# Kernel optimization log

Measured on AMD Instinct MI355X. Metric: run time of the kernel, lower is better.

The kernel has to match this reference:

```python
import jax, jax.numpy as jnp
import numpy as np

B, N, H = 8, 256, 128
EDGE_IN = 2 * H + 1
NODE_IN = 2 * H


def _glorot(key, shape):
    fan_in, fan_out = shape[0], shape[1]
    lim = 1.0 / np.sqrt(fan_in)
    return jax.random.uniform(key, shape, jnp.float32, -lim, lim)


def setup_inputs() -> dict:
    key = jax.random.key(0)
    ks = jax.random.split(key, 12)
    node_state = jax.random.normal(ks[0], (B, N, H), jnp.float32)
    positions = jax.random.normal(ks[1], (B, N, 3), jnp.float32)
    mask = jnp.ones((B, N), jnp.float32)
    # edge_mlp: Linear(2H+1 -> H), SiLU, Linear(H -> H)  (weights stored [in, out])
    We1 = _glorot(ks[2], (EDGE_IN, H)); be1 = _glorot(ks[3], (1, H))[0]
    We2 = _glorot(ks[4], (H, H));       be2 = _glorot(ks[5], (1, H))[0]
    # node_mlp: Linear(2H -> H), SiLU, Linear(H -> H)
    Wn1 = _glorot(ks[6], (NODE_IN, H)); bn1 = _glorot(ks[7], (1, H))[0]
    Wn2 = _glorot(ks[8], (H, H));       bn2 = _glorot(ks[9], (1, H))[0]
    return {"node_state": node_state, "positions": positions, "mask": mask,
            "We1": We1, "be1": be1, "We2": We2, "be2": be2,
            "Wn1": Wn1, "bn1": bn1, "Wn2": Wn2, "bn2": bn2}


def reference(node_state, positions, mask, We1, be1, We2, be2, Wn1, bn1, Wn2, bn2):
    b, n, h = node_state.shape
    # pairwise distances [B, N, N, 1]; safe-sqrt so grad at i==j is 0 (exact fwd)
    rel = positions[:, :, None, :] - positions[:, None, :, :]
    sq = jnp.sum(rel * rel, axis=-1, keepdims=True)
    dist = jnp.where(sq > 0, jnp.sqrt(jnp.where(sq > 0, sq, 1.0)), 0.0)
    # broadcast-concat node features for all pairs -> [B, N, N, 2H+1]
    node_i = jnp.broadcast_to(node_state[:, :, None, :], (b, n, n, h))
    node_j = jnp.broadcast_to(node_state[:, None, :, :], (b, n, n, h))
    edge_input = jnp.concatenate([node_i, node_j, dist], axis=-1)
    edge_msg = jax.nn.silu(edge_input @ We1 + be1) @ We2 + be2  # [B,N,N,H]
    # pairwise validity mask [B, N, N, 1]
    edge_mask = (mask[:, None, :] * mask[:, :, None])[..., None]
    edge_msg = edge_msg * edge_mask
    # masked mean over j
    denom = jnp.clip(jnp.sum(edge_mask, axis=2), 1.0, None)  # [B,N,1]
    aggregated = jnp.sum(edge_msg, axis=2) / denom           # [B,N,H]
    node_in = jnp.concatenate([node_state, aggregated], axis=-1)
    updated = jax.nn.silu(node_in @ Wn1 + bn1) @ Wn2 + bn2
    return node_state + updated * mask[..., None]
```

## Files before the change

kernel.cpp:

```cpp
#include <hip/hip_runtime.h>
#include <hip/hip_bf16.h>
#include <math.h>

#define B_ 8
#define N_ 256
#define H_ 128
#define NODES_ (B_ * N_)

__device__ __forceinline__ float silu_fast(float x) {
    float e = __expf(-x);
    return x * __builtin_amdgcn_rcpf(1.0f + e);
}

__global__ __launch_bounds__(512) void k1(
    const float* __restrict__ node, const float* __restrict__ We1,
    const float* __restrict__ be1, const float* __restrict__ Wn1,
    const float* __restrict__ bn1, const float* __restrict__ mask,
    float* __restrict__ P, float* __restrict__ Q, float* __restrict__ pre)
{
    __shared__ __align__(16) float act[4][128];
    __shared__ __align__(16) float pls[16][4][128];
    const int t = threadIdx.x;
    const int g = blockIdx.x >> 9;
    const int node0 = (blockIdx.x & 511) * 4;

    if (t < 128) {
        int r = t >> 5, col = (t & 31) * 4;
        *(float4*)(&act[r][col]) = *(const float4*)(node + (size_t)(node0 + r) * H_ + col);
    }
    const float* W = (g == 0) ? We1 : (g == 1) ? (We1 + 128 * H_) : Wn1;
    const int kseg = t >> 5;
    const int c0   = (t & 31) * 4;
    __syncthreads();

    float4 w[8];
    const float* Wb = W + (size_t)(kseg * 8) * H_ + c0;
    #pragma unroll
    for (int u = 0; u < 8; ++u) w[u] = *(const float4*)(Wb + u * H_);

    #pragma unroll
    for (int n = 0; n < 4; ++n) {
        float4 a = {0.f, 0.f, 0.f, 0.f};
        #pragma unroll
        for (int u = 0; u < 8; ++u) {
            float v = act[n][kseg * 8 + u];
            a.x = fmaf(v, w[u].x, a.x);
            a.y = fmaf(v, w[u].y, a.y);
            a.z = fmaf(v, w[u].z, a.z);
            a.w = fmaf(v, w[u].w, a.w);
        }
        *(float4*)(&pls[kseg][n][c0]) = a;
    }
    __syncthreads();

    {
        const int n = t >> 7;
        const int c = t & 127;
        float s = 0.f;
        #pragma unroll
        for (int seg = 0; seg < 16; ++seg) s += pls[seg][n][c];
        float* op;
        if (g == 0)      { op = P;   s += be1[c]; }
        else if (g == 1) { op = Q;   s += (mask[node0 + n] - 1.0f) * 1e30f; }
        else             { op = pre; s += bn1[c]; }
        op[(size_t)(node0 + n) * H_ + c] = s;
    }
}

__global__ __launch_bounds__(512, 4) void k2bc(
    const float* __restrict__ P, const float* __restrict__ Q,
    const float* __restrict__ We1, const float* __restrict__ positions,
    const float* __restrict__ mask, const float* __restrict__ pre,
    const float* __restrict__ node,
    const float* __restrict__ We2, const float* __restrict__ be2,
    const float* __restrict__ Wn1, const float* __restrict__ Wn2,
    const float* __restrict__ bn2, float* __restrict__ out)
{
    __shared__ __align__(16) float arena[8192];
    __shared__ __align__(16) float dt[4][256];
    __shared__ float Sls[4][128];
    __shared__ float Tls[4][128];
    __shared__ float cs;
    const int t  = threadIdx.x;
    const int b  = blockIdx.x >> 6;
    const int i0 = (blockIdx.x & 63) * 4;

    {
        const int j    = t & 255;
        const int half = t >> 8;
        const float* pb = positions + b * N_ * 3;
        const float pjx = pb[j * 3 + 0];
        const float pjy = pb[j * 3 + 1];
        const float pjz = pb[j * 3 + 2];
        #pragma unroll
        for (int p = 0; p < 2; ++p) {
            const int il = half * 2 + p;
            float dx = pb[(i0 + il) * 3 + 0] - pjx;
            float dy = pb[(i0 + il) * 3 + 1] - pjy;
            float dz = pb[(i0 + il) * 3 + 2] - pjz;
            float sq = dx * dx + dy * dy + dz * dz;
            dt[il][j] = (sq > 0.f) ? sqrtf(sq) : 0.f;
        }
    }
    if (t < 64) {
        float mv = mask[b * N_ + t] + mask[b * N_ + 64 + t]
                 + mask[b * N_ + 128 + t] + mask[b * N_ + 192 + t];
        #pragma unroll
        for (int off = 32; off >= 1; off >>= 1) mv += __shfl_down(mv, off);
        if (t == 0) cs = mv;
    }

    const int i = t >> 7;
    const int c = t & 127;
    const float wd   = We1[256 * H_ + c];
    const float base = P[(size_t)(b * N_ + i0 + i) * H_ + c];
    const float4* __restrict__ Qg = (const float4*)(Q + (size_t)(b * N_) * H_);

    float4 r0 = Qg[0 * 512 + t];
    float4 r1 = Qg[1 * 512 + t];
    float4 r2 = Qg[2 * 512 + t];
    float4 r3 = Qg[3 * 512 + t];

    float acc = 0.f;
    for (int ch = 0; ch < 4; ++ch) {
        __syncthreads();
        ((float4*)arena)[0 * 512 + t] = r0;
        ((float4*)arena)[1 * 512 + t] = r1;
        ((float4*)arena)[2 * 512 + t] = r2;
        ((float4*)arena)[3 * 512 + t] = r3;
        if (ch < 3) {
            r0 = Qg[(ch + 1) * 2048 + 0 * 512 + t];
            r1 = Qg[(ch + 1) * 2048 + 1 * 512 + t];
            r2 = Qg[(ch + 1) * 2048 + 2 * 512 + t];
            r3 = Qg[(ch + 1) * 2048 + 3 * 512 + t];
        }
        __syncthreads();
        const int j0 = ch * 64;
        #pragma unroll 4
        for (int jw = 0; jw < 64; jw += 4) {
            float4 d4 = *(const float4*)(&dt[i][j0 + jw]);
            #pragma unroll
            for (int u = 0; u < 4; ++u) {
                float q  = arena[(jw + u) * 128 + c];
                float du = (u == 0) ? d4.x : (u == 1) ? d4.y : (u == 2) ? d4.z : d4.w;
                float x  = fmaf(du, wd, base + q);
                float e  = __expf(-x);
                float rr = __builtin_amdgcn_rcpf(1.0f + e);
                acc = fmaf(x, rr, acc);
            }
        }
    }

    const float inv_cnt = __builtin_amdgcn_rcpf(fmaxf(cs, 1.0f));
    const float mi = mask[b * N_ + i0 + i];
    Sls[i][c] = (mi * inv_cnt) * acc;
    __syncthreads();

    float (*pls)[4][128] = (float (*)[4][128])arena;
    const int kseg = t >> 5;
    const int c0   = (t & 31) * 4;

    {
        const float* Wb = We2 + (size_t)(kseg * 8) * H_ + c0;
        float4 w[8];
        #pragma unroll
        for (int u = 0; u < 8; ++u) w[u] = *(const float4*)(Wb + u * H_);
        #pragma unroll
        for (int n = 0; n < 4; ++n) {
            float4 a = {0.f, 0.f, 0.f, 0.f};
            #pragma unroll
            for (int u = 0; u < 8; ++u) {
                float v = Sls[n][kseg * 8 + u];
                a.x = fmaf(v, w[u].x, a.x); a.y = fmaf(v, w[u].y, a.y);
                a.z = fmaf(v, w[u].z, a.z); a.w = fmaf(v, w[u].w, a.w);
            }
            *(float4*)(&pls[kseg][n][c0]) = a;
        }
    }
    __syncthreads();
    {
        float s = 0.f;
        #pragma unroll
        for (int seg = 0; seg < 16; ++seg) s += pls[seg][i][c];
        Tls[i][c] = fmaf(mi, be2[c], s);
    }
    __syncthreads();

    {
        const float* Wb = Wn1 + (size_t)(128 + kseg * 8) * H_ + c0;
        float4 w[8];
        #pragma unroll
        for (int u = 0; u < 8; ++u) w[u] = *(const float4*)(Wb + u * H_);
        #pragma unroll
        for (int n = 0; n < 4; ++n) {
            float4 a = {0.f, 0.f, 0.f, 0.f};
            #pragma unroll
            for (int u = 0; u < 8; ++u) {
                float v = Tls[n][kseg * 8 + u];
                a.x = fmaf(v, w[u].x, a.x); a.y = fmaf(v, w[u].y, a.y);
                a.z = fmaf(v, w[u].z, a.z); a.w = fmaf(v, w[u].w, a.w);
            }
            *(float4*)(&pls[kseg][n][c0]) = a;
        }
    }
    __syncthreads();
    {
        float s = 0.f;
        #pragma unroll
        for (int seg = 0; seg < 16; ++seg) s += pls[seg][i][c];
        Sls[i][c] = silu_fast(pre[(size_t)(b * N_ + i0 + i) * H_ + c] + s);
    }
    __syncthreads();

    {
        const float* Wb = Wn2 + (size_t)(kseg * 8) * H_ + c0;
        float4 w[8];
        #pragma unroll
        for (int u = 0; u < 8; ++u) w[u] = *(const float4*)(Wb + u * H_);
        #pragma unroll
        for (int n = 0; n < 4; ++n) {
            float4 a = {0.f, 0.f, 0.f, 0.f};
            #pragma unroll
            for (int u = 0; u < 8; ++u) {
                float v = Sls[n][kseg * 8 + u];
                a.x = fmaf(v, w[u].x, a.x); a.y = fmaf(v, w[u].y, a.y);
                a.z = fmaf(v, w[u].z, a.z); a.w = fmaf(v, w[u].w, a.w);
            }
            *(float4*)(&pls[kseg][n][c0]) = a;
        }
    }
    __syncthreads();
    {
        float s = 0.f;
        #pragma unroll
        for (int seg = 0; seg < 16; ++seg) s += pls[seg][i][c];
        const size_t idx = (size_t)(b * N_ + i0 + i) * H_ + c;
        out[idx] = node[idx] + mi * (s + bn2[c]);
    }
}

extern "C" void kernel_launch(void* const* d_in, const int* in_sizes, int n_in,
                              void* d_out, int out_size, void* d_ws, size_t ws_size,
                              hipStream_t stream)
{
    const float* node      = (const float*)d_in[0];
    const float* positions = (const float*)d_in[1];
    const float* mask      = (const float*)d_in[2];
    const float* We1       = (const float*)d_in[3];
    const float* be1       = (const float*)d_in[4];
    const float* We2       = (const float*)d_in[5];
    const float* be2       = (const float*)d_in[6];
    const float* Wn1       = (const float*)d_in[7];
    const float* bn1       = (const float*)d_in[8];
    const float* Wn2       = (const float*)d_in[9];
    const float* bn2       = (const float*)d_in[10];
    float* out = (float*)d_out;

    const size_t SZ = (size_t)NODES_ * H_;
    float* P   = (float*)d_ws;
    float* Q   = P + SZ;
    float* pre = Q + SZ;

    k1  <<<1536, 512, 0, stream>>>(node, We1, be1, Wn1, bn1, mask, P, Q, pre);
    k2bc<<<512,  512, 0, stream>>>(P, Q, We1, positions, mask, pre, node,
                                   We2, be2, Wn1, Wn2, bn2, out);
}
```

Measured before the change: 104.3 us.

## Split edge j-range across thread groups and read Q directly from global

Each thread now handles four channels for one node i over a quarter of the j range, loading Q rows as float4 straight from global memory. This replaces the chunked LDS staging loop and its repeated barriers. Partial sums from the four j-quarters are written to LDS and reduced afterwards. The aim is to drop the staging syncs and LDS traffic and raise per-thread ILP. In exchange it relies on cache hits for the repeated global Q reads and adds one partial-sum reduction step.

```diff
diff --git a/kernel.cpp b/kernel.cpp
--- a/kernel.cpp
+++ b/kernel.cpp
@@ -109,56 +109,54 @@
         for (int off = 32; off >= 1; off >>= 1) mv += __shfl_down(mv, off);
         if (t == 0) cs = mv;
     }
-
+    __syncthreads();
+
+    const int jq = t >> 7;
+    const int il = (t >> 5) & 3;
+    const int c0 = (t & 31) * 4;
+    float4 base4 = *(const float4*)(P + (size_t)(b * N_ + i0 + il) * H_ + c0);
+    float4 wd4   = *(const float4*)(We1 + (size_t)(256) * H_ + c0);
+    const float* __restrict__ Qb = Q + (size_t)(b * N_ + jq * 64) * H_ + c0;
+
+    float4 acc = {0.f, 0.f, 0.f, 0.f};
+    #pragma unroll 4
+    for (int jw = 0; jw < 16; ++jw) {
+        float4 d4 = *(const float4*)(&dt[il][jq * 64 + jw * 4]);
+        #pragma unroll
+        for (int u = 0; u < 4; ++u) {
+            float4 q4 = *(const float4*)(Qb + (size_t)(jw * 4 + u) * H_);
+            float d = (u == 0) ? d4.x : (u == 1) ? d4.y : (u == 2) ? d4.z : d4.w;
+            float x0 = fmaf(d, wd4.x, base4.x + q4.x);
+            float x1 = fmaf(d, wd4.y, base4.y + q4.y);
+            float x2 = fmaf(d, wd4.z, base4.z + q4.z);
+            float x3 = fmaf(d, wd4.w, base4.w + q4.w);
+            float r0 = __builtin_amdgcn_rcpf(1.0f + __expf(-x0));
+            float r1 = __builtin_amdgcn_rcpf(1.0f + __expf(-x1));
+            float r2 = __builtin_amdgcn_rcpf(1.0f + __expf(-x2));
+            float r3 = __builtin_amdgcn_rcpf(1.0f + __expf(-x3));
+            acc.x = fmaf(x0, r0, acc.x);
+            acc.y = fmaf(x1, r1, acc.y);
+            acc.z = fmaf(x2, r2, acc.z);
+            acc.w = fmaf(x3, r3, acc.w);
+        }
+    }
+
+    float (*parts)[4][128] = (float (*)[4][128])arena;
+    *(float4*)(&parts[jq][il][c0]) = acc;
+    __syncthreads();
     const int i = t >> 7;
     const int c = t & 127;
-    const float wd   = We1[256 * H_ + c];
-    const float base = P[(size_t)(b * N_ + i0 + i) * H_ + c];
-    const float4* __restrict__ Qg = (const float4*)(Q + (size_t)(b * N_) * H_);
-
-    float4 r0 = Qg[0 * 512 + t];
-    float4 r1 = Qg[1 * 512 + t];
-    float4 r2 = Qg[2 * 512 + t];
-    float4 r3 = Qg[3 * 512 + t];
-
-    float acc = 0.f;
-    for (int ch = 0; ch < 4; ++ch) {
-        __syncthreads();
-        ((float4*)arena)[0 * 512 + t] = r0;
-        ((float4*)arena)[1 * 512 + t] = r1;
-        ((float4*)arena)[2 * 512 + t] = r2;
-        ((float4*)arena)[3 * 512 + t] = r3;
-        if (ch < 3) {
-            r0 = Qg[(ch + 1) * 2048 + 0 * 512 + t];
-            r1 = Qg[(ch + 1) * 2048 + 1 * 512 + t];
-            r2 = Qg[(ch + 1) * 2048 + 2 * 512 + t];
-            r3 = Qg[(ch + 1) * 2048 + 3 * 512 + t];
-        }
-        __syncthreads();
-        const int j0 = ch * 64;
-        #pragma unroll 4
-        for (int jw = 0; jw < 64; jw += 4) {
-            float4 d4 = *(const float4*)(&dt[i][j0 + jw]);
-            #pragma unroll
-            for (int u = 0; u < 4; ++u) {
-                float q  = arena[(jw + u) * 128 + c];
-                float du = (u == 0) ? d4.x : (u == 1) ? d4.y : (u == 2) ? d4.z : d4.w;
-                float x  = fmaf(du, wd, base + q);
-                float e  = __expf(-x);
-                float rr = __builtin_amdgcn_rcpf(1.0f + e);
-                acc = fmaf(x, rr, acc);
-            }
-        }
-    }
-
     const float inv_cnt = __builtin_amdgcn_rcpf(fmaxf(cs, 1.0f));
     const float mi = mask[b * N_ + i0 + i];
-    Sls[i][c] = (mi * inv_cnt) * acc;
+    {
+        float s = (parts[0][i][c] + parts[1][i][c])
+                + (parts[2][i][c] + parts[3][i][c]);
+        Sls[i][c] = (mi * inv_cnt) * s;
+    }
     __syncthreads();
 
     float (*pls)[4][128] = (float (*)[4][128])arena;
     const int kseg = t >> 5;
-    const int c0   = (t & 31) * 4;
 
     {
         const float* Wb = We2 + (size_t)(kseg * 8) * H_ + c0;
```

Result: no change. 104.5 us (+0.2%).
